# Optimization experiments

Hardware: AMD Instinct MI355X
Metric: run time of the kernel (lower is better)

## Reference

```python
import jax, jax.numpy as jnp
import numpy as np


def setup_inputs() -> dict:
    key = jax.random.key(0)
    k1, k2 = jax.random.split(key)
    B, N, D = 4, 2048, 1024
    context = jax.random.normal(k1, (B, N, D), dtype=jnp.float32)
    # Dense(embedding_dim*3): kernel [D, 3D], bias [3D] (glorot-ish scale)
    W_qkv = jax.random.normal(k2, (D, 3 * D), dtype=jnp.float32) * (1.0 / np.sqrt(D))
    b_qkv = jnp.zeros((3 * D,), dtype=jnp.float32)
    return {"context": context, "W_qkv": W_qkv, "b_qkv": b_qkv}


def reference(context, W_qkv, b_qkv):
    B, N, D = context.shape
    qkv = context @ W_qkv + b_qkv                       # [B, N, 3D]
    q, k, v = jnp.split(qkv, 3, axis=-1)                # each [B, N, D]
    scores = jnp.einsum("bnd,bmd->bnm", q, k)           # [B, N, N]
    # Faithful quirk: original divides by sqrt(scores.shape[-1]) == sqrt(N)
    scores = scores / jnp.asarray(np.sqrt(N), dtype=scores.dtype)
    causal = jnp.tril(jnp.ones((N, N), dtype=jnp.float32))  # lower-triangular
    scores = jnp.where(causal == 0, -jnp.inf, scores)
    probs = jax.nn.softmax(scores, axis=-1)             # [B, N, N]
    out = jnp.einsum("bnm,bmd->bnd", probs, v)          # [B, N, D]
    return out
```

## Files before the change

### kernel.cpp

```cpp
#include <hip/hip_runtime.h>
#include <cstdint>
#include <cstddef>


typedef __attribute__((ext_vector_type(8))) __bf16 bf16x8;
typedef __attribute__((ext_vector_type(4))) float f32x4;

__device__ inline unsigned short f2bf(float f) {
  unsigned u = __float_as_uint(f);
  u = (u + 0x7FFFu + ((u >> 16) & 1u)) >> 16;
  return (unsigned short)u;
}

__device__ inline void gld16(const void* g, void* l) {
  __builtin_amdgcn_global_load_lds(
      (const __attribute__((address_space(1))) unsigned int*)g,
      (__attribute__((address_space(3))) unsigned int*)l, 16, 0, 0);
}


__device__ inline void stage_Ahalf(const unsigned short* Agb, int k0,
                                   unsigned short* Abuf, int half,
                                   int wave, int lrow, int lcol) {
#pragma unroll
  for (int i = 0; i < 2; i++) {
    const int c = wave * 2 + i;
    const int rg = ((c >> 3) << 7) + ((c & 7) << 3) + (half << 6);
    gld16(Agb + (size_t)(rg + lrow) * 1024 + k0 + lcol, Abuf + rg * 64);
  }
}

__device__ inline void stage_Bhalf(const unsigned short* Bgb, int k0,
                                   unsigned short* Bbuf, int half,
                                   int wave, int lrow, int lcol) {
#pragma unroll
  for (int i = 0; i < 2; i++) {
    const int c = wave * 2 + i;
    const int rg = ((c >> 2) << 6) + ((c & 3) << 3) + (half << 5);
    gld16(Bgb + (size_t)(rg + lrow) * 1024 + k0 + lcol, Bbuf + rg * 64);
  }
}

__device__ inline void read_Ahalf(const unsigned short* buf, int wm, int half,
                                  int lane, bf16x8 (&a)[4][2]) {
#pragma unroll
  for (int ks = 0; ks < 2; ks++) {
    const int csw = ((((ks << 2) + (lane >> 4)) ^ (lane & 7)) << 3);
#pragma unroll
    for (int mi = 0; mi < 4; mi++) {
      const int R = wm * 128 + half * 64 + mi * 16 + (lane & 15);
      a[mi][ks] = *(const bf16x8*)&buf[R * 64 + csw];
    }
  }
}

__device__ inline void read_Bhalf(const unsigned short* buf, int wn, int half,
                                  int lane, bf16x8 (&b)[2][2]) {
#pragma unroll
  for (int ks = 0; ks < 2; ks++) {
    const int csw = ((((ks << 2) + (lane >> 4)) ^ (lane & 7)) << 3);
#pragma unroll
    for (int nj = 0; nj < 2; nj++) {
      const int R = wn * 64 + half * 32 + nj * 16 + (lane & 15);
      b[nj][ks] = *(const bf16x8*)&buf[R * 64 + csw];
    }
  }
}

__device__ inline void mma_quad(const bf16x8 (&a)[4][2], const bf16x8 (&b)[2][2],
                                f32x4 (&acc)[8][4], const int ah, const int bh) {
#pragma unroll
  for (int ks = 0; ks < 2; ks++)
#pragma unroll
    for (int mi = 0; mi < 4; mi++)
#pragma unroll
      for (int nj = 0; nj < 2; nj++)
        acc[ah * 4 + mi][bh * 2 + nj] = __builtin_amdgcn_mfma_f32_16x16x32_bf16(
            b[nj][ks], a[mi][ks], acc[ah * 4 + mi][bh * 2 + nj], 0, 0, 0);
}

#define QKV_MFMA_PHASE(AFRAG, BFRAG, AH, BH)        \
  __builtin_amdgcn_s_barrier();                     \
  asm volatile("s_waitcnt lgkmcnt(0)" ::: "memory"); \
  __builtin_amdgcn_sched_barrier(0);                \
  __builtin_amdgcn_s_setprio(1);                    \
  mma_quad(AFRAG, BFRAG, acc, AH, BH);              \
  __builtin_amdgcn_s_setprio(0);                    \
  __builtin_amdgcn_sched_barrier(0);                \
  __builtin_amdgcn_s_barrier()

template <bool STG, int C4, int C8>
__device__ inline void qkv_iter(const unsigned short* Agb, const unsigned short* Bgb,
                                int k1, int k2, int k3,
                                unsigned short* sA, unsigned short* sB,
                                int wave, int lane, int wm, int wn,
                                f32x4 (&acc)[8][4]) {
  const int lrow = lane >> 3, lcol = ((lane & 7) ^ lrow) * 8;
  unsigned short *A0 = sA, *A1 = sA + 16384, *B0 = sB, *B1 = sB + 16384;
  bf16x8 aLo[4][2], aHi[4][2], bLo[2][2], bHi[2][2];

  read_Ahalf(A0, wm, 0, lane, aLo);
  read_Bhalf(B0, wn, 0, lane, bLo);
  stage_Ahalf(Agb, k1, A1, 1, wave, lrow, lcol);
  QKV_MFMA_PHASE(aLo, bLo, 0, 0);
  read_Bhalf(B0, wn, 1, lane, bHi);
  if (STG) stage_Ahalf(Agb, k2, A0, 0, wave, lrow, lcol);
  QKV_MFMA_PHASE(aLo, bHi, 0, 1);
  read_Ahalf(A0, wm, 1, lane, aHi);
  if (STG) stage_Bhalf(Bgb, k2, B0, 0, wave, lrow, lcol);
  QKV_MFMA_PHASE(aHi, bHi, 1, 1);
  if (STG) stage_Bhalf(Bgb, k2, B0, 1, wave, lrow, lcol);
  if constexpr (C4 >= 0)
    asm volatile("s_waitcnt vmcnt(%0)" ::"i"(C4) : "memory");
  QKV_MFMA_PHASE(aHi, bLo, 1, 0);
  read_Ahalf(A1, wm, 0, lane, aLo);
  read_Bhalf(B1, wn, 0, lane, bLo);
  if (STG) stage_Ahalf(Agb, k2, A0, 1, wave, lrow, lcol);
  QKV_MFMA_PHASE(aLo, bLo, 0, 0);
  read_Bhalf(B1, wn, 1, lane, bHi);
  if (STG) stage_Ahalf(Agb, k3, A1, 0, wave, lrow, lcol);
  QKV_MFMA_PHASE(aLo, bHi, 0, 1);
  read_Ahalf(A1, wm, 1, lane, aHi);
  if (STG) stage_Bhalf(Bgb, k3, B1, 0, wave, lrow, lcol);
  QKV_MFMA_PHASE(aHi, bHi, 1, 1);
  if (STG) stage_Bhalf(Bgb, k3, B1, 1, wave, lrow, lcol);
  if constexpr (C8 >= 0)
    asm volatile("s_waitcnt vmcnt(%0)" ::"i"(C8) : "memory");
  QKV_MFMA_PHASE(aHi, bLo, 1, 0);
}

__global__ __launch_bounds__(512, 2) void k_gemm_qkv(
    const unsigned short* __restrict__ A, const unsigned short* __restrict__ Wt,
    const float* __restrict__ bias, unsigned short* __restrict__ qk,
    unsigned short* __restrict__ vT) {
  __shared__ unsigned short sA[2 * 16384];
  __shared__ unsigned short sB[2 * 16384];
  const int bid = blockIdx.y * 12 + blockIdx.x;
  const int swz = (bid & 7) * 48 + (bid >> 3);
  const int nb = swz % 12, mb = swz / 12;
  const int tN0 = nb * 256, tM0 = mb * 256;
  const unsigned short* Agb = A + (size_t)tM0 * 1024;
  const unsigned short* Bgb = Wt + (size_t)tN0 * 1024;
  const int lane = threadIdx.x & 63, wave = threadIdx.x >> 6;
  const int wm = wave >> 2, wn = wave & 3;
  const int lrow = lane >> 3, lcol = ((lane & 7) ^ lrow) * 8;

  f32x4 acc[8][4];
#pragma unroll
  for (int mi = 0; mi < 8; mi++)
#pragma unroll
    for (int nj = 0; nj < 4; nj++) acc[mi][nj] = (f32x4)(0.f);

  stage_Ahalf(Agb, 0, sA, 0, wave, lrow, lcol);
  stage_Bhalf(Bgb, 0, sB, 0, wave, lrow, lcol);
  stage_Bhalf(Bgb, 0, sB, 1, wave, lrow, lcol);
  stage_Ahalf(Agb, 0, sA, 1, wave, lrow, lcol);
  stage_Ahalf(Agb, 64, sA + 16384, 0, wave, lrow, lcol);
  stage_Bhalf(Bgb, 64, sB + 16384, 0, wave, lrow, lcol);
  stage_Bhalf(Bgb, 64, sB + 16384, 1, wave, lrow, lcol);
  asm volatile("s_waitcnt vmcnt(6)" ::: "memory");
  __builtin_amdgcn_s_barrier();

  for (int i = 0; i < 7; i++)
    qkv_iter<true, 6, 6>(Agb, Bgb, (2 * i + 1) * 64, (2 * i + 2) * 64,
                         (2 * i + 3) * 64, sA, sB, wave, lane, wm, wn, acc);
  qkv_iter<false, 0, -1>(Agb, Bgb, 15 * 64, 0, 0, sA, sB, wave, lane, wm, wn, acc);

  const int l16 = lane & 15, rq = lane >> 4;
  int m0 = tM0 + wm * 128;
  asm volatile("" : "+v"(m0));
  if (tN0 < 2048) {
#pragma unroll
    for (int mi = 0; mi < 8; mi++) {
      const int m = m0 + mi * 16 + l16;
#pragma unroll
      for (int nj = 0; nj < 4; nj++) {
        const int n = tN0 + wn * 64 + nj * 16 + rq * 4;
        const float4 bv = *(const float4*)&bias[n];
        ushort4 o;
        o.x = f2bf(acc[mi][nj][0] + bv.x);
        o.y = f2bf(acc[mi][nj][1] + bv.y);
        o.z = f2bf(acc[mi][nj][2] + bv.z);
        o.w = f2bf(acc[mi][nj][3] + bv.w);
        *(ushort4*)&qk[(size_t)m * 2048 + n] = o;
      }
    }
  } else {
    const int d0b = tN0 - 2048 + wn * 64;
#pragma unroll
    for (int mi = 0; mi < 8; mi++) {
      const int m = m0 + mi * 16 + l16;
      const int b = m >> 11, ns = m & 2047;
#pragma unroll
      for (int nj = 0; nj < 4; nj++) {
        const int d0 = d0b + nj * 16 + rq * 4;
        const float4 bv = *(const float4*)&bias[2048 + d0];
#pragma unroll
        for (int r = 0; r < 4; r++)
          vT[((size_t)(b * 1024 + d0 + r)) * 2048 + ns] =
              f2bf(acc[mi][nj][r] + ((const float*)&bv)[r]);
      }
    }
  }
}

__device__ inline void compute_tiles64(const unsigned short* As, const unsigned short* Bs,
                                       int lane, int ry, int rx, f32x4 acc[4][2]) {
#pragma unroll
  for (int kk = 0; kk < 64; kk += 32) {
    const int cbase = (kk >> 3) + (lane >> 4);
    const int csw = ((cbase ^ (lane & 7)) << 3);
    bf16x8 a[4], b[2];
#pragma unroll
    for (int mi = 0; mi < 4; mi++)
      a[mi] = *(const bf16x8*)&As[(ry + mi * 16 + (lane & 15)) * 64 + csw];
#pragma unroll
    for (int nj = 0; nj < 2; nj++)
      b[nj] = *(const bf16x8*)&Bs[(rx + nj * 16 + (lane & 15)) * 64 + csw];
#pragma unroll
    for (int mi = 0; mi < 4; mi++)
#pragma unroll
      for (int nj = 0; nj < 2; nj++)
        acc[mi][nj] = __builtin_amdgcn_mfma_f32_16x16x32_bf16(b[nj], a[mi], acc[mi][nj], 0, 0, 0);
  }
}

__device__ inline void mma_mainloop64(unsigned short* As, unsigned short* Bs,
                                      const unsigned short* Abase, long strideA,
                                      const unsigned short* Bbase, long strideB,
                                      int kIters, f32x4 acc[4][2]) {
  const int lane = threadIdx.x & 63, wave = threadIdx.x >> 6;
  const int ry = (wave >> 1) * 64, rx = (wave & 1) * 32;
  const int lrow = lane >> 3;
  const int lcol = ((lane & 7) ^ lrow) * 8;
#pragma unroll
  for (int mi = 0; mi < 4; mi++)
#pragma unroll
    for (int nj = 0; nj < 2; nj++) acc[mi][nj] = (f32x4)(0.f);
  for (int kt = 0; kt < kIters; kt++) {
    const int k0 = kt * 64;
    __syncthreads();
#pragma unroll
    for (int c = 0; c < 4; c++) {
      const int q = wave * 4 + c;
      const int row = q * 8 + lrow;
      gld16(Abase + (size_t)row * strideA + k0 + lcol, &As[q * 512]);
    }
#pragma unroll
    for (int c = 0; c < 2; c++) {
      const int q = wave * 2 + c;
      const int row = q * 8 + lrow;
      gld16(Bbase + (size_t)row * strideB + k0 + lcol, &Bs[q * 512]);
    }
    __syncthreads();
    compute_tiles64(As, Bs, lane, ry, rx, acc);
  }
}


__global__ void k_convert(const float* __restrict__ x, unsigned short* __restrict__ y, int n4) {
  int i = blockIdx.x * blockDim.x + threadIdx.x;
  if (i >= n4) return;
  float4 v = ((const float4*)x)[i];
  ushort4 o;
  o.x = f2bf(v.x); o.y = f2bf(v.y); o.z = f2bf(v.z); o.w = f2bf(v.w);
  ((ushort4*)y)[i] = o;
}

__global__ void k_transpose_w(const float* __restrict__ W, unsigned short* __restrict__ Wt) {
  __shared__ unsigned short sm[64 * 65];
  const int n0 = blockIdx.x * 64;
  const int k0 = blockIdx.y * 64;
  for (int i = threadIdx.x; i < 4096; i += 256) {
    int r = i >> 6, c = i & 63;
    sm[c * 65 + r] = f2bf(W[(size_t)(k0 + r) * 3072 + n0 + c]);
  }
  __syncthreads();
  for (int i = threadIdx.x; i < 4096; i += 256) {
    int r = i >> 6, c = i & 63;
    Wt[(size_t)(n0 + r) * 1024 + k0 + c] = sm[r * 65 + c];
  }
}


__global__ __launch_bounds__(256) void k_scores(const unsigned short* __restrict__ qk,
                                                unsigned short* __restrict__ P,
                                                float* __restrict__ l, float scale) {
  __shared__ unsigned short As[128 * 64];
  __shared__ unsigned short Bs[64 * 64];
  const int t = blockIdx.x, b = blockIdx.z;
  int qb = (int)((sqrtf(4.0f * (float)t + 1.0f) - 1.0f) * 0.5f);
  while (qb * (qb + 1) > t) qb--;
  while ((qb + 1) * (qb + 2) <= t) qb++;
  const int kb2 = t - qb * (qb + 1);
  f32x4 acc[4][2];
  const unsigned short* Aq = qk + ((size_t)(b * 2048 + qb * 128)) * 2048;
  const unsigned short* Bk = qk + ((size_t)(b * 2048 + kb2 * 64)) * 2048 + 1024;
  mma_mainloop64(As, Bs, Aq, 2048, Bk, 2048, 16, acc);
  const int lane = threadIdx.x & 63, wave = threadIdx.x >> 6;
  const int ry = (wave >> 1) * 64, rx = (wave & 1) * 32;
  const int l16 = lane & 15, rq = lane >> 4;
  unsigned short* Pb = P + ((size_t)(b * 2048 + qb * 128)) * 2048 + (size_t)kb2 * 64;
  float* lb = l + b * 2048 + qb * 128;
#pragma unroll
  for (int mi = 0; mi < 4; mi++) {
    const int m_local = ry + mi * 16 + l16;
    const int qi = qb * 128 + m_local;
    float rowpart = 0.f;
#pragma unroll
    for (int nj = 0; nj < 2; nj++) {
      const int n_base = rx + nj * 16 + rq * 4;
      ushort4 o;
      float p;
#pragma unroll
      for (int r = 0; r < 4; r++) {
        const int kj = kb2 * 64 + n_base + r;
        p = (kj <= qi) ? __expf(acc[mi][nj][r] * scale) : 0.f;
        rowpart += p;
        ((unsigned short*)&o)[r] = f2bf(p);
      }
      *(ushort4*)&Pb[(size_t)m_local * 2048 + n_base] = o;
    }
    rowpart += __shfl_xor(rowpart, 16, 64);
    rowpart += __shfl_xor(rowpart, 32, 64);
    if (rq == 0) atomicAdd(&lb[m_local], rowpart);
  }
}

__global__ __launch_bounds__(256) void k_pv(const unsigned short* __restrict__ P,
                                            const unsigned short* __restrict__ vT,
                                            const float* __restrict__ l,
                                            float* __restrict__ out) {
  __shared__ unsigned short As[128 * 64];
  __shared__ unsigned short Bs[64 * 64];
  const int db2 = blockIdx.x, b = blockIdx.z;
  int qb = blockIdx.y;
  if (b & 2) qb = 15 - qb;
  f32x4 acc[4][2];
  const unsigned short* Ap = P + ((size_t)(b * 2048 + qb * 128)) * 2048;
  const unsigned short* Bv = vT + ((size_t)(b * 1024 + db2 * 64)) * 2048;
  mma_mainloop64(As, Bs, Ap, 2048, Bv, 2048, (qb + 1) * 2, acc);
  const int lane = threadIdx.x & 63, wave = threadIdx.x >> 6;
  const int ry = (wave >> 1) * 64, rx = (wave & 1) * 32;
  const int l16 = lane & 15, rq = lane >> 4;
  const float* lb = l + b * 2048 + qb * 128;
  float* ob = out + ((size_t)(b * 2048 + qb * 128)) * 1024 + db2 * 64;
#pragma unroll
  for (int mi = 0; mi < 4; mi++) {
    const int m_local = ry + mi * 16 + l16;
    const float inv = 1.0f / lb[m_local];
#pragma unroll
    for (int nj = 0; nj < 2; nj++) {
      const int n_base = rx + nj * 16 + rq * 4;
      float4 o;
      o.x = acc[mi][nj][0] * inv;
      o.y = acc[mi][nj][1] * inv;
      o.z = acc[mi][nj][2] * inv;
      o.w = acc[mi][nj][3] * inv;
      *(float4*)&ob[(size_t)m_local * 1024 + n_base] = o;
    }
  }
}


extern "C" void kernel_launch(void* const* d_in, const int* in_sizes, int n_in,
                              void* d_out, int out_size, void* d_ws, size_t ws_size,
                              hipStream_t stream) {
  const float* ctx  = (const float*)d_in[0];
  const float* W    = (const float*)d_in[1];
  const float* bias = (const float*)d_in[2];
  float* out = (float*)d_out;

  char* ws = (char*)d_ws;
  unsigned short* Actx = (unsigned short*)(ws + 0);
  unsigned short* Wt   = (unsigned short*)(ws + 16777216);
  unsigned short* qk   = (unsigned short*)(ws + 23068672);
  unsigned short* vT   = (unsigned short*)(ws + 56623104);
  unsigned short* P    = (unsigned short*)(ws + 73400320);
  float*          lsum = (float*)(ws + 106954752);

  hipMemsetAsync(lsum, 0, 4 * 2048 * sizeof(float), stream);
  k_convert<<<8192, 256, 0, stream>>>(ctx, Actx, (8192 * 1024) / 4);
  k_transpose_w<<<dim3(48, 16), 256, 0, stream>>>(W, Wt);
  k_gemm_qkv<<<dim3(12, 32), 512, 0, stream>>>(Actx, Wt, bias, qk, vT);
  k_scores<<<dim3(272, 1, 4), 256, 0, stream>>>(qk, P, lsum, 0.022097086912079608f);
  k_pv<<<dim3(16, 16, 4), 256, 0, stream>>>(P, vT, lsum, out);
}
```

Measured before the change: 255.4 us.

## Split QKV GEMM into small-tile and pipelined big-tile kernels with LDS address-space reads

The QKV projection is now split across two launches. A new simple 128x128-tile kernel covers the first 4096 rows with 768 blocks. The existing 256x256 pipelined kernel covers the remaining 4096 rows with 192 blocks and an adjusted block swizzle. The pipelined kernel also reads LDS through explicit address-space-3 pointers and adds partial lgkmcnt waits so fragment reads can overlap the barrier. The likely aim is better CU utilisation and less wave quantisation across the 256 CUs, at the cost of an extra launch and a slower, non-pipelined small-tile kernel for half the work.

```diff
diff --git a/kernel.cpp b/kernel.cpp
--- a/kernel.cpp
+++ b/kernel.cpp
@@ -5,6 +5,7 @@
 
 typedef __attribute__((ext_vector_type(8))) __bf16 bf16x8;
 typedef __attribute__((ext_vector_type(4))) float f32x4;
+#define AS3 __attribute__((address_space(3)))
 
 __device__ inline unsigned short f2bf(float f) {
   unsigned u = __float_as_uint(f);
@@ -15,7 +16,7 @@
 __device__ inline void gld16(const void* g, void* l) {
   __builtin_amdgcn_global_load_lds(
       (const __attribute__((address_space(1))) unsigned int*)g,
-      (__attribute__((address_space(3))) unsigned int*)l, 16, 0, 0);
+      (AS3 unsigned int*)l, 16, 0, 0);
 }
 
 
@@ -41,7 +42,7 @@
   }
 }
 
-__device__ inline void read_Ahalf(const unsigned short* buf, int wm, int half,
+__device__ inline void read_Ahalf(const AS3 unsigned short* buf, int wm, int half,
                                   int lane, bf16x8 (&a)[4][2]) {
 #pragma unroll
   for (int ks = 0; ks < 2; ks++) {
@@ -49,12 +50,12 @@
 #pragma unroll
     for (int mi = 0; mi < 4; mi++) {
       const int R = wm * 128 + half * 64 + mi * 16 + (lane & 15);
-      a[mi][ks] = *(const bf16x8*)&buf[R * 64 + csw];
-    }
-  }
-}
-
-__device__ inline void read_Bhalf(const unsigned short* buf, int wn, int half,
+      a[mi][ks] = *(const AS3 bf16x8*)&buf[R * 64 + csw];
+    }
+  }
+}
+
+__device__ inline void read_Bhalf(const AS3 unsigned short* buf, int wn, int half,
                                   int lane, bf16x8 (&b)[2][2]) {
 #pragma unroll
   for (int ks = 0; ks < 2; ks++) {
@@ -62,7 +63,7 @@
 #pragma unroll
     for (int nj = 0; nj < 2; nj++) {
       const int R = wn * 64 + half * 32 + nj * 16 + (lane & 15);
-      b[nj][ks] = *(const bf16x8*)&buf[R * 64 + csw];
+      b[nj][ks] = *(const AS3 bf16x8*)&buf[R * 64 + csw];
     }
   }
 }
@@ -92,58 +93,65 @@
 template <bool STG, int C4, int C8>
 __device__ inline void qkv_iter(const unsigned short* Agb, const unsigned short* Bgb,
                                 int k1, int k2, int k3,
+                                const AS3 unsigned short* A0, const AS3 unsigned short* A1,
+                                const AS3 unsigned short* B0, const AS3 unsigned short* B1,
                                 unsigned short* sA, unsigned short* sB,
                                 int wave, int lane, int wm, int wn,
                                 f32x4 (&acc)[8][4]) {
   const int lrow = lane >> 3, lcol = ((lane & 7) ^ lrow) * 8;
-  unsigned short *A0 = sA, *A1 = sA + 16384, *B0 = sB, *B1 = sB + 16384;
   bf16x8 aLo[4][2], aHi[4][2], bLo[2][2], bHi[2][2];
 
   read_Ahalf(A0, wm, 0, lane, aLo);
   read_Bhalf(B0, wn, 0, lane, bLo);
-  stage_Ahalf(Agb, k1, A1, 1, wave, lrow, lcol);
+  stage_Ahalf(Agb, k1, sA + 16384, 1, wave, lrow, lcol);
+  asm volatile("s_waitcnt lgkmcnt(8)" ::: "memory");
   QKV_MFMA_PHASE(aLo, bLo, 0, 0);
   read_Bhalf(B0, wn, 1, lane, bHi);
-  if (STG) stage_Ahalf(Agb, k2, A0, 0, wave, lrow, lcol);
+  if (STG) stage_Ahalf(Agb, k2, sA, 0, wave, lrow, lcol);
   QKV_MFMA_PHASE(aLo, bHi, 0, 1);
   read_Ahalf(A0, wm, 1, lane, aHi);
-  if (STG) stage_Bhalf(Bgb, k2, B0, 0, wave, lrow, lcol);
+  if (STG) stage_Bhalf(Bgb, k2, sB, 0, wave, lrow, lcol);
   QKV_MFMA_PHASE(aHi, bHi, 1, 1);
-  if (STG) stage_Bhalf(Bgb, k2, B0, 1, wave, lrow, lcol);
+  if (STG) stage_Bhalf(Bgb, k2, sB, 1, wave, lrow, lcol);
   if constexpr (C4 >= 0)
     asm volatile("s_waitcnt vmcnt(%0)" ::"i"(C4) : "memory");
   QKV_MFMA_PHASE(aHi, bLo, 1, 0);
   read_Ahalf(A1, wm, 0, lane, aLo);
   read_Bhalf(B1, wn, 0, lane, bLo);
-  if (STG) stage_Ahalf(Agb, k2, A0, 1, wave, lrow, lcol);
+  if (STG) stage_Ahalf(Agb, k2, sA, 1, wave, lrow, lcol);
+  asm volatile("s_waitcnt lgkmcnt(8)" ::: "memory");
   QKV_MFMA_PHASE(aLo, bLo, 0, 0);
   read_Bhalf(B1, wn, 1, lane, bHi);
-  if (STG) stage_Ahalf(Agb, k3, A1, 0, wave, lrow, lcol);
+  if (STG) stage_Ahalf(Agb, k3, sA + 16384, 0, wave, lrow, lcol);
   QKV_MFMA_PHASE(aLo, bHi, 0, 1);
   read_Ahalf(A1, wm, 1, lane, aHi);
-  if (STG) stage_Bhalf(Bgb, k3, B1, 0, wave, lrow, lcol);
+  if (STG) stage_Bhalf(Bgb, k3, sB + 16384, 0, wave, lrow, lcol);
   QKV_MFMA_PHASE(aHi, bHi, 1, 1);
-  if (STG) stage_Bhalf(Bgb, k3, B1, 1, wave, lrow, lcol);
+  if (STG) stage_Bhalf(Bgb, k3, sB + 16384, 1, wave, lrow, lcol);
   if constexpr (C8 >= 0)
     asm volatile("s_waitcnt vmcnt(%0)" ::"i"(C8) : "memory");
   QKV_MFMA_PHASE(aHi, bLo, 1, 0);
 }
 
-__global__ __launch_bounds__(512, 2) void k_gemm_qkv(
+__global__ __launch_bounds__(512, 2) void k_gemm_qkv_p(
     const unsigned short* __restrict__ A, const unsigned short* __restrict__ Wt,
     const float* __restrict__ bias, unsigned short* __restrict__ qk,
     unsigned short* __restrict__ vT) {
   __shared__ unsigned short sA[2 * 16384];
   __shared__ unsigned short sB[2 * 16384];
   const int bid = blockIdx.y * 12 + blockIdx.x;
-  const int swz = (bid & 7) * 48 + (bid >> 3);
+  const int swz = (bid & 7) * 24 + (bid >> 3);
   const int nb = swz % 12, mb = swz / 12;
-  const int tN0 = nb * 256, tM0 = mb * 256;
+  const int tN0 = nb * 256, tM0 = 4096 + mb * 256;
   const unsigned short* Agb = A + (size_t)tM0 * 1024;
   const unsigned short* Bgb = Wt + (size_t)tN0 * 1024;
   const int lane = threadIdx.x & 63, wave = threadIdx.x >> 6;
   const int wm = wave >> 2, wn = wave & 3;
   const int lrow = lane >> 3, lcol = ((lane & 7) ^ lrow) * 8;
+  const AS3 unsigned short* A0 = (const AS3 unsigned short*)sA;
+  const AS3 unsigned short* A1 = A0 + 16384;
+  const AS3 unsigned short* B0 = (const AS3 unsigned short*)sB;
+  const AS3 unsigned short* B1 = B0 + 16384;
 
   f32x4 acc[8][4];
 #pragma unroll
@@ -163,8 +171,10 @@
 
   for (int i = 0; i < 7; i++)
     qkv_iter<true, 6, 6>(Agb, Bgb, (2 * i + 1) * 64, (2 * i + 2) * 64,
-                         (2 * i + 3) * 64, sA, sB, wave, lane, wm, wn, acc);
-  qkv_iter<false, 0, -1>(Agb, Bgb, 15 * 64, 0, 0, sA, sB, wave, lane, wm, wn, acc);
+                         (2 * i + 3) * 64, A0, A1, B0, B1, sA, sB,
+                         wave, lane, wm, wn, acc);
+  qkv_iter<false, 0, -1>(Agb, Bgb, 15 * 64, 0, 0, A0, A1, B0, B1, sA, sB,
+                         wave, lane, wm, wn, acc);
 
   const int l16 = lane & 15, rq = lane >> 4;
   int m0 = tM0 + wm * 128;
@@ -194,6 +204,106 @@
 #pragma unroll
       for (int nj = 0; nj < 4; nj++) {
         const int d0 = d0b + nj * 16 + rq * 4;
+        const float4 bv = *(const float4*)&bias[2048 + d0];
+#pragma unroll
+        for (int r = 0; r < 4; r++)
+          vT[((size_t)(b * 1024 + d0 + r)) * 2048 + ns] =
+              f2bf(acc[mi][nj][r] + ((const float*)&bv)[r]);
+      }
+    }
+  }
+}
+
+__device__ inline void compute_tiles(const unsigned short* As, const unsigned short* Bs,
+                                     int lane, int ry, int rx, f32x4 acc[4][4]) {
+#pragma unroll
+  for (int kk = 0; kk < 64; kk += 32) {
+    const int cbase = (kk >> 3) + (lane >> 4);
+    const int csw = ((cbase ^ (lane & 7)) << 3);
+    bf16x8 a[4], b[4];
+#pragma unroll
+    for (int mi = 0; mi < 4; mi++)
+      a[mi] = *(const bf16x8*)&As[(ry + mi * 16 + (lane & 15)) * 64 + csw];
+#pragma unroll
+    for (int nj = 0; nj < 4; nj++)
+      b[nj] = *(const bf16x8*)&Bs[(rx + nj * 16 + (lane & 15)) * 64 + csw];
+#pragma unroll
+    for (int mi = 0; mi < 4; mi++)
+#pragma unroll
+      for (int nj = 0; nj < 4; nj++)
+        acc[mi][nj] = __builtin_amdgcn_mfma_f32_16x16x32_bf16(b[nj], a[mi], acc[mi][nj], 0, 0, 0);
+  }
+}
+
+__device__ inline void mma_mainloop(unsigned short* As, unsigned short* Bs,
+                                    const unsigned short* Abase, long strideA,
+                                    const unsigned short* Bbase, long strideB,
+                                    int kIters, f32x4 acc[4][4]) {
+  const int lane = threadIdx.x & 63, wave = threadIdx.x >> 6;
+  const int ry = (wave >> 1) * 64, rx = (wave & 1) * 64;
+  const int lrow = lane >> 3;
+  const int lcol = ((lane & 7) ^ lrow) * 8;
+#pragma unroll
+  for (int mi = 0; mi < 4; mi++)
+#pragma unroll
+    for (int nj = 0; nj < 4; nj++) acc[mi][nj] = (f32x4)(0.f);
+  for (int kt = 0; kt < kIters; kt++) {
+    const int k0 = kt * 64;
+    __syncthreads();
+#pragma unroll
+    for (int c = 0; c < 4; c++) {
+      const int q = wave * 4 + c;
+      const int row = q * 8 + lrow;
+      gld16(Abase + (size_t)row * strideA + k0 + lcol, &As[q * 512]);
+      gld16(Bbase + (size_t)row * strideB + k0 + lcol, &Bs[q * 512]);
+    }
+    __syncthreads();
+    compute_tiles(As, Bs, lane, ry, rx, acc);
+  }
+}
+
+__global__ __launch_bounds__(256) void k_gemm_qkv_s(
+    const unsigned short* __restrict__ A, const unsigned short* __restrict__ Wt,
+    const float* __restrict__ bias, unsigned short* __restrict__ qk,
+    unsigned short* __restrict__ vT) {
+  __shared__ unsigned short As[128 * 64];
+  __shared__ unsigned short Bs[128 * 64];
+  f32x4 acc[4][4];
+  const int bx = blockIdx.x;
+  const int tM0 = blockIdx.y * 128;
+  const int feat0 = bx * 128;
+  mma_mainloop(As, Bs, A + (size_t)tM0 * 1024, 1024,
+               Wt + (size_t)feat0 * 1024, 1024, 16, acc);
+  int tM0v = tM0;
+  asm volatile("" : "+v"(tM0v));
+  const int lane = threadIdx.x & 63, wave = threadIdx.x >> 6;
+  const int ry = (wave >> 1) * 64, rx = (wave & 1) * 64;
+  const int l16 = lane & 15, rq = lane >> 4;
+  if (bx < 16) {
+#pragma unroll
+    for (int mi = 0; mi < 4; mi++) {
+      const int m = tM0v + ry + mi * 16 + l16;
+#pragma unroll
+      for (int nj = 0; nj < 4; nj++) {
+        const int n = feat0 + rx + nj * 16 + rq * 4;
+        const float4 bv = *(const float4*)&bias[n];
+        ushort4 o;
+        o.x = f2bf(acc[mi][nj][0] + bv.x);
+        o.y = f2bf(acc[mi][nj][1] + bv.y);
+        o.z = f2bf(acc[mi][nj][2] + bv.z);
+        o.w = f2bf(acc[mi][nj][3] + bv.w);
+        *(ushort4*)&qk[(size_t)m * 2048 + n] = o;
+      }
+    }
+  } else {
+    const int tNv = feat0 - 2048;
+#pragma unroll
+    for (int mi = 0; mi < 4; mi++) {
+      const int m = tM0v + ry + mi * 16 + l16;
+      const int b = m >> 11, ns = m & 2047;
+#pragma unroll
+      for (int nj = 0; nj < 4; nj++) {
+        const int d0 = tNv + rx + nj * 16 + rq * 4;
         const float4 bv = *(const float4*)&bias[2048 + d0];
 #pragma unroll
         for (int r = 0; r < 4; r++)
@@ -382,7 +492,8 @@
   hipMemsetAsync(lsum, 0, 4 * 2048 * sizeof(float), stream);
   k_convert<<<8192, 256, 0, stream>>>(ctx, Actx, (8192 * 1024) / 4);
   k_transpose_w<<<dim3(48, 16), 256, 0, stream>>>(W, Wt);
-  k_gemm_qkv<<<dim3(12, 32), 512, 0, stream>>>(Actx, Wt, bias, qk, vT);
+  k_gemm_qkv_s<<<dim3(24, 32), 256, 0, stream>>>(Actx, Wt, bias, qk, vT);
+  k_gemm_qkv_p<<<dim3(12, 16), 512, 0, stream>>>(Actx, Wt, bias, qk, vT);
   k_scores<<<dim3(272, 1, 4), 256, 0, stream>>>(qk, P, lsum, 0.022097086912079608f);
   k_pv<<<dim3(16, 16, 4), 256, 0, stream>>>(P, vT, lsum, out);
 }
```

New measurement: 270.7 us. 1.06x slower.
